# Kernel optimization log

Hardware: AMD Instinct MI355X
Metric: run time of the kernel (lower is better)

Reference implementation:

```python
import jax, jax.numpy as jnp
import numpy as np

EPS = 1e-12  # torch.nn.functional.normalize eps


def setup_inputs() -> dict:
    key = jax.random.key(0)
    k1, k2 = jax.random.split(key)
    B, S, H, A = 16, 2048, 1024, 1024
    x = jax.random.normal(k1, (B, S, H), dtype=jnp.float32)
    group_by = jnp.sort(jax.random.randint(k2, (B, S), 0, A), axis=-1)
    return {"x": x, "group_by": group_by, "agg_step": A}


def reference(x, group_by, agg_step):
    # pos_proj[b, a, s] = (group_by[b, s] == a); negative group ids never match.
    pos = jnp.arange(agg_step)[None, :, None] == group_by[:, None, :]  # (B, A, S) bool
    w = pos.astype(x.dtype)
    # L1-normalize over source steps (torch F.normalize p=1 with eps clamp);
    # empty groups -> all-zero row -> zero output, matching original semantics.
    w = w / jnp.maximum(w.sum(axis=-1, keepdims=True), EPS)
    # mean aggregation as batched matmul, same as pos_proj_weight.bmm(x)
    return jnp.einsum('bas,bsh->bah', w, x)  # (B, A, H)
```

## Files before the change

### kernel.cpp

```cpp
#include <hip/hip_runtime.h>


constexpr int AG = 2;

typedef float v4f __attribute__((ext_vector_type(4)));

__global__ __launch_bounds__(256) void seg_bounds_kernel(
    const int* __restrict__ gb,
    int2*      __restrict__ bounds,
    int S, int A) {
  const int b = blockIdx.y;
  const int a = blockIdx.x * blockDim.x + threadIdx.x;
  if (a >= A) return;
  const int* __restrict__ g = gb + (size_t)b * S;
  int lo = 0, hi = S;
  while (lo < hi) { int m = (lo + hi) >> 1; if (g[m] < a) lo = m + 1; else hi = m; }
  const int start = lo;
  hi = S;
  while (lo < hi) { int m = (lo + hi) >> 1; if (g[m] <= a) lo = m + 1; else hi = m; }
  bounds[(size_t)b * A + a] = make_int2(start, lo);
}

__global__ __launch_bounds__(256) void seq_group_agg_kernel(
    const float* __restrict__ x,
    const int2*  __restrict__ bounds,
    float*       __restrict__ out,
    int S, int H4, int A) {
  const int b  = blockIdx.y;
  const int a0 = blockIdx.x * AG;

  int2 se[AG];
#pragma unroll
  for (int j = 0; j < AG; ++j) se[j] = bounds[(size_t)b * A + a0 + j];

  const v4f* __restrict__ xb = (const v4f*)x + (size_t)b * S * H4;
  const int h4 = threadIdx.x;

  v4f acc[AG];
  float scale[AG];
#pragma unroll
  for (int j = 0; j < AG; ++j) {
    const int cnt = se[j].y - se[j].x;
    scale[j] = (cnt > 0) ? (1.0f / (float)cnt) : 0.0f;
    acc[j] = (v4f)(0.0f);
  }
#pragma unroll
  for (int j = 0; j < AG; ++j) {
    for (int s = se[j].x; s < se[j].y; ++s) {
      acc[j] += __builtin_nontemporal_load(xb + (size_t)s * H4 + h4);
    }
  }
  v4f* __restrict__ ob = (v4f*)out + ((size_t)b * A + a0) * H4 + h4;
#pragma unroll
  for (int j = 0; j < AG; ++j) {
    __builtin_nontemporal_store(acc[j] * scale[j], ob + (size_t)j * H4);
  }
}

extern "C" void kernel_launch(void* const* d_in, const int* in_sizes, int n_in,
                              void* d_out, int out_size, void* d_ws, size_t ws_size,
                              hipStream_t stream) {
  const float* x  = (const float*)d_in[0];
  const int*   gb = (const int*)d_in[1];
  float*       out = (float*)d_out;

  const int BS = in_sizes[1];
  const int H  = in_sizes[0] / BS;
  const int A  = 1024;
  const int B  = (out_size / H) / A;
  const int S  = BS / B;

  int2* bounds = (int2*)d_ws;

  dim3 g1((A + 255) / 256, B);
  seg_bounds_kernel<<<g1, 256, 0, stream>>>(gb, bounds, S, A);

  dim3 g2(A / AG, B);
  seq_group_agg_kernel<<<g2, 256, 0, stream>>>(x, bounds, out, S, H / 4, A);
}
```

Before: 212.1 us.

## Stream contiguous segment range per block with prefetch and end-only bounds

The bounds kernel now does a single upper-bound binary search per group, storing only segment ends; starts come from the previous group's end. The aggregation kernel stages AG+1 ends in shared memory. It then walks the whole contiguous row range for 4 groups in one loop, with a one-ahead software prefetch, flushing the scaled accumulator at each segment boundary. This halves the search work, doubles groups per block and keeps a single serial load stream, at the cost of data-dependent branching inside the inner loop.

```diff
diff --git a/kernel.cpp b/kernel.cpp
--- a/kernel.cpp
+++ b/kernel.cpp
@@ -1,59 +1,71 @@
 #include <hip/hip_runtime.h>
 
 
-constexpr int AG = 2;
+constexpr int AG = 4;
 
 typedef float v4f __attribute__((ext_vector_type(4)));
 
-__global__ __launch_bounds__(256) void seg_bounds_kernel(
+__global__ __launch_bounds__(256) void seg_ends_kernel(
     const int* __restrict__ gb,
-    int2*      __restrict__ bounds,
+    int*       __restrict__ ends,
     int S, int A) {
   const int b = blockIdx.y;
   const int a = blockIdx.x * blockDim.x + threadIdx.x;
   if (a >= A) return;
   const int* __restrict__ g = gb + (size_t)b * S;
   int lo = 0, hi = S;
-  while (lo < hi) { int m = (lo + hi) >> 1; if (g[m] < a) lo = m + 1; else hi = m; }
-  const int start = lo;
-  hi = S;
   while (lo < hi) { int m = (lo + hi) >> 1; if (g[m] <= a) lo = m + 1; else hi = m; }
-  bounds[(size_t)b * A + a] = make_int2(start, lo);
+  ends[(size_t)b * A + a] = lo;
 }
 
 __global__ __launch_bounds__(256) void seq_group_agg_kernel(
     const float* __restrict__ x,
-    const int2*  __restrict__ bounds,
+    const int*   __restrict__ ends,
     float*       __restrict__ out,
     int S, int H4, int A) {
   const int b  = blockIdx.y;
   const int a0 = blockIdx.x * AG;
 
-  int2 se[AG];
-#pragma unroll
-  for (int j = 0; j < AG; ++j) se[j] = bounds[(size_t)b * A + a0 + j];
+  __shared__ int e[AG + 1];
+  if (threadIdx.x <= AG) {
+    const int idx = a0 - 1 + (int)threadIdx.x;
+    e[threadIdx.x] = (idx < 0) ? 0 : ends[(size_t)b * A + idx];
+  }
+  __syncthreads();
 
-  const v4f* __restrict__ xb = (const v4f*)x + (size_t)b * S * H4;
   const int h4 = threadIdx.x;
+  const v4f* __restrict__ xb = (const v4f*)x + (size_t)b * S * H4 + h4;
+  v4f* __restrict__ ob = (v4f*)out + ((size_t)b * A + a0) * H4 + h4;
 
-  v4f acc[AG];
-  float scale[AG];
-#pragma unroll
-  for (int j = 0; j < AG; ++j) {
-    const int cnt = se[j].y - se[j].x;
-    scale[j] = (cnt > 0) ? (1.0f / (float)cnt) : 0.0f;
-    acc[j] = (v4f)(0.0f);
+  const int sBeg = e[0];
+  const int sEnd = e[AG];
+
+  int j = 0;
+  int y = e[1];
+  int seg_start = sBeg;
+
+  while (j < AG && y == sBeg) {
+    __builtin_nontemporal_store((v4f)(0.0f), ob + (size_t)j * H4);
+    ++j;
+    y = (j < AG) ? e[j + 1] : -1;
   }
-#pragma unroll
-  for (int j = 0; j < AG; ++j) {
-    for (int s = se[j].x; s < se[j].y; ++s) {
-      acc[j] += __builtin_nontemporal_load(xb + (size_t)s * H4 + h4);
+
+  v4f acc = (v4f)(0.0f);
+  v4f nxt = (v4f)(0.0f);
+  if (sBeg < sEnd) nxt = __builtin_nontemporal_load(xb + (size_t)sBeg * H4);
+  for (int s = sBeg; s < sEnd; ++s) {
+    const v4f cur = nxt;
+    if (s + 1 < sEnd) nxt = __builtin_nontemporal_load(xb + (size_t)(s + 1) * H4);
+    acc += cur;
+    while (j < AG && s + 1 == y) {
+      const int cnt = y - seg_start;
+      const float sc = (cnt > 0) ? 1.0f / (float)cnt : 0.0f;
+      __builtin_nontemporal_store(acc * sc, ob + (size_t)j * H4);
+      acc = (v4f)(0.0f);
+      seg_start = y;
+      ++j;
+      y = (j < AG) ? e[j + 1] : -1;
     }
-  }
-  v4f* __restrict__ ob = (v4f*)out + ((size_t)b * A + a0) * H4 + h4;
-#pragma unroll
-  for (int j = 0; j < AG; ++j) {
-    __builtin_nontemporal_store(acc[j] * scale[j], ob + (size_t)j * H4);
   }
 }
 
@@ -70,11 +82,11 @@
   const int B  = (out_size / H) / A;
   const int S  = BS / B;
 
-  int2* bounds = (int2*)d_ws;
+  int* ends = (int*)d_ws;
 
   dim3 g1((A + 255) / 256, B);
-  seg_bounds_kernel<<<g1, 256, 0, stream>>>(gb, bounds, S, A);
+  seg_ends_kernel<<<g1, 256, 0, stream>>>(gb, ends, S, A);
 
   dim3 g2(A / AG, B);
-  seq_group_agg_kernel<<<g2, 256, 0, stream>>>(x, bounds, out, S, H / 4, A);
+  seq_group_agg_kernel<<<g2, 256, 0, stream>>>(x, ends, out, S, H / 4, A);
 }
```

Measured after the change: 212.6 us. Within noise of the previous version (+0.2%).
